# Kernel optimization log

Measured on AMD Instinct MI355X. Metric: run time of the kernel, lower is better.

## Reference

```python
import jax, jax.numpy as jnp
import numpy as np

B, N = 8, 2048
IN_F, MID1, HID, MID2, OUT_F = 128, 128, 128, 128, 128
BIG = 9e15  # matches torch's 9000000000000000.0 additive mask constant


def _linear_params(key, out_d, in_d):
    # torch Linear layout: W is [out, in]
    kw, kb = jax.random.split(key)
    w = jax.random.normal(kw, (out_d, in_d), jnp.float32) * (1.0 / np.sqrt(in_d))
    b = jax.random.normal(kb, (out_d,), jnp.float32) * 0.01
    return w, b


def setup_inputs() -> dict:
    key = jax.random.key(0)
    ks = jax.random.split(key, 16)
    h = jax.random.normal(ks[0], (B, N, IN_F), jnp.float32)
    adj = jax.random.randint(ks[1], (B, N, N), 0, 2).astype(jnp.float32)
    vae2_fetures = jax.random.normal(ks[2], (B, N, OUT_F), jnp.float32)
    Wv1, bv1 = _linear_params(ks[3], MID1, IN_F)
    Wk1, bk1 = _linear_params(ks[4], MID1, IN_F)
    Wq1, bq1 = _linear_params(ks[5], MID1, IN_F)
    Wo1, bo1 = _linear_params(ks[6], HID, MID1)
    Wv2, bv2 = _linear_params(ks[7], MID2, HID)
    Wk2, bk2 = _linear_params(ks[8], MID2, HID)
    Wq2, bq2 = _linear_params(ks[9], MID2, HID)
    Wo2, bo2 = _linear_params(ks[10], OUT_F, MID2)
    Wf, bf = _linear_params(ks[11], OUT_F, 2 * OUT_F)
    return {
        "h": h, "adj": adj, "vae2_fetures": vae2_fetures,
        "Wv1": Wv1, "bv1": bv1, "Wk1": Wk1, "bk1": bk1, "Wq1": Wq1, "bq1": bq1,
        "Wo1": Wo1, "bo1": bo1,
        "Wv2": Wv2, "bv2": bv2, "Wk2": Wk2, "bk2": bk2, "Wq2": Wq2, "bq2": bq2,
        "Wo2": Wo2, "bo2": bo2, "Wf": Wf, "bf": bf,
    }


def _lin(x, W, b):
    return jnp.einsum('bnd,od->bno', x, W) + b


def _masked_att_block(x, adj, Wq, bq, Wk, bk, Wv, bv):
    v = jax.nn.relu(_lin(x, Wv, bv))          # [B,N,D]
    q = jax.nn.relu(_lin(x, Wq, bq))          # [B,N,D]
    k = jax.nn.relu(_lin(x, Wk, bk))          # [B,N,D]
    s = jnp.einsum('bnd,bmd->bnm', q, k)       # [B,N,N]
    masked = s * adj - BIG * (1.0 - adj)       # multiplicative + additive mask
    att = jax.nn.softmax(masked, axis=-1)
    return jnp.einsum('bnm,bmd->bnd', att, v)


def reference(h, adj, vae2_fetures,
              Wv1, bv1, Wk1, bk1, Wq1, bq1, Wo1, bo1,
              Wv2, bv2, Wk2, bk2, Wq2, bq2, Wo2, bo2,
              Wf, bf):
    f1 = _masked_att_block(h, adj, Wq1, bq1, Wk1, bk1, Wv1, bv1)
    f1 = _lin(f1, Wo1, bo1)                    # [B,N,HID]
    f2 = _masked_att_block(f1, adj, Wq2, bq2, Wk2, bk2, Wv2, bv2)
    f2 = _lin(f2, Wo2, bo2)                    # [B,N,OUT_F]
    f3 = jnp.concatenate([f2, vae2_fetures], axis=2)
    return _lin(f3, Wf, bf)                    # [B,N,OUT_F]
```

## Files before the change

kernel.cpp:

```cpp
#include <hip/hip_runtime.h>

typedef short s16x8 __attribute__((ext_vector_type(8)));
typedef float f32x4 __attribute__((ext_vector_type(4)));
typedef unsigned short u16x4v __attribute__((ext_vector_type(4)));

#define NSPLIT 4
#define NROWS 16384
#define MSHIFT 44.0f

__device__ __forceinline__ unsigned short f2bf(float f) {
  union { float fl; unsigned int i; } v; v.fl = f;
  unsigned int x = v.i;
  x += 0x7fffu + ((x >> 16) & 1u);
  return (unsigned short)(x >> 16);
}
__device__ __forceinline__ s16x8 load8_bf16(const unsigned short* p) {
  return *(const s16x8*)p;
}
__device__ __forceinline__ s16x8 load8_f32(const float* p) {
  float4 a = *(const float4*)p;
  float4 b = *(const float4*)(p + 4);
  s16x8 r;
  r[0] = (short)f2bf(a.x); r[1] = (short)f2bf(a.y);
  r[2] = (short)f2bf(a.z); r[3] = (short)f2bf(a.w);
  r[4] = (short)f2bf(b.x); r[5] = (short)f2bf(b.y);
  r[6] = (short)f2bf(b.z); r[7] = (short)f2bf(b.w);
  return r;
}
__device__ __forceinline__ int vperm(int nn) {
  return (nn & ~31) | (((nn >> 2) & 3) << 3) | (((nn >> 4) & 1) << 2);
}

template <int MODE>
__device__ __forceinline__ void qkv_body(
    const float* __restrict__ X, const float* __restrict__ W,
    const float* __restrict__ bias, unsigned short* __restrict__ out)
{
  const int t = threadIdx.x;
  const int w = t >> 6;
  const int lane = t & 63;
  const int l15 = lane & 15;
  const int quad = lane >> 4;
  const int mbase = blockIdx.x * 16;

  s16x8 a[4];
  const float* ar = X + (size_t)(mbase + l15) * 128;
#pragma unroll
  for (int ks = 0; ks < 4; ++ks) a[ks] = load8_f32(ar + ks * 32 + quad * 8);

#pragma unroll
  for (int nt = 0; nt < 2; ++nt) {
    const int n = (w * 2 + nt) * 16 + l15;
    f32x4 acc = {0.f, 0.f, 0.f, 0.f};
    const float* wr = W + (size_t)n * 128;
#pragma unroll
    for (int ks = 0; ks < 4; ++ks)
      acc = __builtin_amdgcn_mfma_f32_16x16x32_bf16(
          a[ks], load8_f32(wr + ks * 32 + quad * 8), acc, 0, 0, 0);
    const float bv = bias[n];
    if (MODE == 0) {
#pragma unroll
      for (int r = 0; r < 4; ++r)
        out[(size_t)(mbase + quad * 4 + r) * 128 + n] = f2bf(fmaxf(acc[r] + bv, 0.f));
    } else {
      const int b  = mbase >> 11;
      const int nn = (mbase & 2047) + quad * 4;
      u16x4v pk;
#pragma unroll
      for (int r = 0; r < 4; ++r) pk[r] = f2bf(fmaxf(acc[r] + bv, 0.f));
      *(u16x4v*)(out + (size_t)(b * 128 + n) * 2048 + vperm(nn)) = pk;
    }
  }
}

__global__ __launch_bounds__(256) void qkv1_kernel(
    const float* __restrict__ x,
    const float* __restrict__ Wq, const float* __restrict__ bq, unsigned short* __restrict__ oq,
    const float* __restrict__ Wk, const float* __restrict__ bk, unsigned short* __restrict__ ok,
    const float* __restrict__ Wv, const float* __restrict__ bv, unsigned short* __restrict__ ovt)
{
  if (blockIdx.y == 0)      qkv_body<0>(x, Wq, bq, oq);
  else if (blockIdx.y == 1) qkv_body<0>(x, Wk, bk, ok);
  else                      qkv_body<1>(x, Wv, bv, ovt);
}

template <bool PACK>
__global__ __launch_bounds__(256, 2) void attn_kernel(
    const unsigned short* __restrict__ Q,
    const unsigned short* __restrict__ K,
    const unsigned short* __restrict__ VT,
    const float* __restrict__ ADJ,
    unsigned long long* __restrict__ MASK,
    float* __restrict__ pO, float* __restrict__ pl)
{
  __shared__ __align__(16) unsigned short kbuf[64][136];
  __shared__ __align__(16) unsigned short vbuf[128][72];

  const int t = threadIdx.x;
  const int w = t >> 6;
  const int lane = t & 63;
  const int l15 = lane & 15;
  const int quad = lane >> 4;

  const int gq0 = blockIdx.x * 128;
  const int b   = gq0 >> 11;
  const int q0  = gq0 & 2047;
  const int wq0 = q0 + w * 32;
  const int kc0 = blockIdx.y * (2048 / NSPLIT);

  const unsigned short* Kb  = K  + (size_t)(b * 2048) * 128;
  const unsigned short* VTb = VT + (size_t)(b * 128) * 2048;
  const float* ADJb = ADJ + (size_t)b * 2048 * 2048;
  unsigned long long* Mb = MASK + (size_t)b * 2048 * 32;

  s16x8 qf[2][4];
#pragma unroll
  for (int mt = 0; mt < 2; ++mt) {
    const unsigned short* qrow = Q + (size_t)(gq0 + w * 32 + mt * 16 + l15) * 128;
#pragma unroll
    for (int ks = 0; ks < 4; ++ks) qf[mt][ks] = load8_bf16(qrow + ks * 32 + quad * 8);
  }

  s16x8 ones;
#pragma unroll
  for (int i = 0; i < 8; ++i) ones[i] = (short)0x3F80;

  f32x4 accO[2][8];
  f32x4 accL[2];
#pragma unroll
  for (int mt = 0; mt < 2; ++mt) {
    accL[mt] = (f32x4){0.f, 0.f, 0.f, 0.f};
#pragma unroll
    for (int dt = 0; dt < 8; ++dt) accO[mt][dt] = (f32x4){0.f, 0.f, 0.f, 0.f};
  }

  s16x8 kr[4], vr[4];
#pragma unroll
  for (int i = 0; i < 4; ++i) {
    int slot = i * 256 + t;
    kr[i] = load8_bf16(Kb + (size_t)(kc0 + (slot >> 4)) * 128 + (slot & 15) * 8);
    vr[i] = load8_bf16(VTb + (size_t)(slot >> 3) * 2048 + kc0 + (slot & 7) * 8);
  }

  for (int kc = kc0; kc < kc0 + 2048 / NSPLIT; kc += 64) {
    __syncthreads();
#pragma unroll
    for (int i = 0; i < 4; ++i) {
      int slot = i * 256 + t;
      *(s16x8*)&kbuf[slot >> 4][(slot & 15) * 8] = kr[i];
      *(s16x8*)&vbuf[slot >> 3][(slot & 7) * 8]  = vr[i];
    }
    __syncthreads();

    unsigned long long mw[2];
    float4 a4[2][4];
    if (PACK) {
#pragma unroll
      for (int mt = 0; mt < 2; ++mt)
#pragma unroll
        for (int nt = 0; nt < 4; ++nt)
          a4[mt][nt] = *(const float4*)(
              ADJb + (size_t)(wq0 + mt * 16 + l15) * 2048 + kc + nt * 16 + quad * 4);
    } else {
#pragma unroll
      for (int mt = 0; mt < 2; ++mt)
        mw[mt] = Mb[(size_t)(wq0 + mt * 16 + l15) * 32 + (kc >> 6)];
    }

    if (kc + 64 < kc0 + 2048 / NSPLIT) {
#pragma unroll
      for (int i = 0; i < 4; ++i) {
        int slot = i * 256 + t;
        kr[i] = load8_bf16(Kb + (size_t)(kc + 64 + (slot >> 4)) * 128 + (slot & 15) * 8);
        vr[i] = load8_bf16(VTb + (size_t)(slot >> 3) * 2048 + (kc + 64) + (slot & 7) * 8);
      }
    }

    f32x4 sv[2][4];
#pragma unroll
    for (int nt = 0; nt < 4; ++nt) {
      sv[0][nt] = (f32x4){0.f, 0.f, 0.f, 0.f};
      sv[1][nt] = (f32x4){0.f, 0.f, 0.f, 0.f};
#pragma unroll
      for (int ks = 0; ks < 4; ++ks) {
        s16x8 kf = *(const s16x8*)&kbuf[nt * 16 + l15][ks * 32 + quad * 8];
        sv[0][nt] = __builtin_amdgcn_mfma_f32_16x16x32_bf16(kf, qf[0][ks], sv[0][nt], 0, 0, 0);
        sv[1][nt] = __builtin_amdgcn_mfma_f32_16x16x32_bf16(kf, qf[1][ks], sv[1][nt], 0, 0, 0);
      }
    }

    float p[2][4][4];
    if (PACK) {
#pragma unroll
      for (int mt = 0; mt < 2; ++mt) {
        unsigned long long word = 0;
#pragma unroll
        for (int nt = 0; nt < 4; ++nt) {
          unsigned int nib = 0;
#pragma unroll
          for (int r = 0; r < 4; ++r) {
            float av = (r == 0) ? a4[mt][nt].x : (r == 1) ? a4[mt][nt].y
                     : (r == 2) ? a4[mt][nt].z : a4[mt][nt].w;
            bool keep = (av != 0.f);
            float e = __expf(sv[mt][nt][r] - MSHIFT);
            p[mt][nt][r] = keep ? e : 0.f;
            nib |= (keep ? 1u : 0u) << r;
          }
          word |= (unsigned long long)nib << (nt * 16 + quad * 4);
        }
        word |= __shfl_xor(word, 16, 64);
        word |= __shfl_xor(word, 32, 64);
        if (quad == 0)
          Mb[(size_t)(wq0 + mt * 16 + l15) * 32 + (kc >> 6)] = word;
      }
    } else {
#pragma unroll
      for (int mt = 0; mt < 2; ++mt)
#pragma unroll
        for (int nt = 0; nt < 4; ++nt)
#pragma unroll
          for (int r = 0; r < 4; ++r) {
            float e = __expf(sv[mt][nt][r] - MSHIFT);
            p[mt][nt][r] = ((mw[mt] >> (nt * 16 + quad * 4 + r)) & 1ull) ? e : 0.f;
          }
    }

    s16x8 pf[2][2];
#pragma unroll
    for (int mt = 0; mt < 2; ++mt)
#pragma unroll
      for (int ks = 0; ks < 2; ++ks) {
        s16x8 v;
#pragma unroll
        for (int j = 0; j < 4; ++j) {
          v[j]     = (short)f2bf(p[mt][2 * ks][j]);
          v[j + 4] = (short)f2bf(p[mt][2 * ks + 1][j]);
        }
        pf[mt][ks] = v;
      }

#pragma unroll
    for (int mt = 0; mt < 2; ++mt)
#pragma unroll
      for (int ks = 0; ks < 2; ++ks)
        accL[mt] = __builtin_amdgcn_mfma_f32_16x16x32_bf16(ones, pf[mt][ks], accL[mt], 0, 0, 0);

#pragma unroll
    for (int dt = 0; dt < 8; ++dt) {
#pragma unroll
      for (int ks = 0; ks < 2; ++ks) {
        s16x8 vf = *(const s16x8*)&vbuf[dt * 16 + l15][ks * 32 + quad * 8];
        accO[0][dt] = __builtin_amdgcn_mfma_f32_16x16x32_bf16(vf, pf[0][ks], accO[0][dt], 0, 0, 0);
        accO[1][dt] = __builtin_amdgcn_mfma_f32_16x16x32_bf16(vf, pf[1][ks], accO[1][dt], 0, 0, 0);
      }
    }
  }

  float* pOs = pO + (size_t)blockIdx.y * NROWS * 128;
#pragma unroll
  for (int mt = 0; mt < 2; ++mt) {
    const int qg = gq0 + w * 32 + mt * 16 + l15;
#pragma unroll
    for (int dt = 0; dt < 8; ++dt)
      *(f32x4*)(pOs + (size_t)qg * 128 + dt * 16 + quad * 4) = accO[mt][dt];
  }
  if (quad == 0) {
#pragma unroll
    for (int mt = 0; mt < 2; ++mt)
      pl[blockIdx.y * NROWS + gq0 + w * 32 + mt * 16 + l15] = accL[mt][0];
  }
}

__device__ __forceinline__ void combine_splits(
    const float* __restrict__ pO, const float* __restrict__ pl, int grow0,
    unsigned short (*At)[136])
{
  const int t = threadIdx.x;
  const int row = t >> 4;
  const int col8 = (t & 15) * 8;
  const int grow = grow0 + row;
  float lsum = 0.f;
#pragma unroll
  for (int s = 0; s < NSPLIT; ++s) lsum += pl[s * NROWS + grow];
  const float inv = (lsum > 0.f) ? 1.f / lsum : 0.f;
  float acc8[8];
#pragma unroll
  for (int i = 0; i < 8; ++i) acc8[i] = 0.f;
#pragma unroll
  for (int s = 0; s < NSPLIT; ++s) {
    const float* p = pO + (size_t)s * NROWS * 128 + (size_t)grow * 128 + col8;
    float4 x0 = *(const float4*)p;
    float4 x1 = *(const float4*)(p + 4);
    acc8[0] += x0.x; acc8[1] += x0.y; acc8[2] += x0.z; acc8[3] += x0.w;
    acc8[4] += x1.x; acc8[5] += x1.y; acc8[6] += x1.z; acc8[7] += x1.w;
  }
#pragma unroll
  for (int i = 0; i < 8; ++i) At[row][col8 + i] = f2bf(acc8[i] * inv);
}

__global__ __launch_bounds__(256) void redqkv_kernel(
    const float* __restrict__ pO, const float* __restrict__ pl,
    const float* __restrict__ Wo, const float* __restrict__ bo,
    const float* __restrict__ Wq, const float* __restrict__ bq, unsigned short* __restrict__ oq,
    const float* __restrict__ Wk, const float* __restrict__ bk, unsigned short* __restrict__ ok,
    const float* __restrict__ Wv, const float* __restrict__ bv, unsigned short* __restrict__ ovt)
{
  __shared__ __align__(16) unsigned short At[16][136];
  __shared__ __align__(16) unsigned short Bt[16][136];
  const int t = threadIdx.x;
  const int grow0 = blockIdx.x * 16;

  combine_splits(pO, pl, grow0, At);
  __syncthreads();

  const int w = t >> 6;
  const int lane = t & 63;
  const int l15 = lane & 15;
  const int quad = lane >> 4;

  s16x8 a[4];
#pragma unroll
  for (int ks = 0; ks < 4; ++ks) a[ks] = *(const s16x8*)&At[l15][ks * 32 + quad * 8];
#pragma unroll
  for (int nt = 0; nt < 2; ++nt) {
    const int n = (w * 2 + nt) * 16 + l15;
    f32x4 acc = {0.f, 0.f, 0.f, 0.f};
    const float* wr = Wo + (size_t)n * 128;
#pragma unroll
    for (int ks = 0; ks < 4; ++ks)
      acc = __builtin_amdgcn_mfma_f32_16x16x32_bf16(
          a[ks], load8_f32(wr + ks * 32 + quad * 8), acc, 0, 0, 0);
    const float bv_ = bo[n];
#pragma unroll
    for (int r = 0; r < 4; ++r) Bt[quad * 4 + r][n] = f2bf(acc[r] + bv_);
  }
  __syncthreads();

  s16x8 a2[4];
#pragma unroll
  for (int ks = 0; ks < 4; ++ks) a2[ks] = *(const s16x8*)&Bt[l15][ks * 32 + quad * 8];

#pragma unroll
  for (int which = 0; which < 3; ++which) {
    const float* W = (which == 0) ? Wq : (which == 1) ? Wk : Wv;
    const float* bb = (which == 0) ? bq : (which == 1) ? bk : bv;
    unsigned short* out = (which == 0) ? oq : (which == 1) ? ok : ovt;
#pragma unroll
    for (int nt = 0; nt < 2; ++nt) {
      const int n = (w * 2 + nt) * 16 + l15;
      f32x4 acc = {0.f, 0.f, 0.f, 0.f};
      const float* wr = W + (size_t)n * 128;
#pragma unroll
      for (int ks = 0; ks < 4; ++ks)
        acc = __builtin_amdgcn_mfma_f32_16x16x32_bf16(
            a2[ks], load8_f32(wr + ks * 32 + quad * 8), acc, 0, 0, 0);
      const float bv_ = bb[n];
      if (which < 2) {
#pragma unroll
        for (int r = 0; r < 4; ++r)
          out[(size_t)(grow0 + quad * 4 + r) * 128 + n] = f2bf(fmaxf(acc[r] + bv_, 0.f));
      } else {
        const int b  = grow0 >> 11;
        const int nn = (grow0 & 2047) + quad * 4;
        u16x4v pk;
#pragma unroll
        for (int r = 0; r < 4; ++r) pk[r] = f2bf(fmaxf(acc[r] + bv_, 0.f));
        *(u16x4v*)(out + (size_t)(b * 128 + n) * 2048 + vperm(nn)) = pk;
      }
    }
  }
}

__global__ __launch_bounds__(256) void redfinal_kernel(
    const float* __restrict__ pO, const float* __restrict__ pl,
    const float* __restrict__ Wo, const float* __restrict__ bo,
    const float* __restrict__ Wf, const float* __restrict__ bff,
    const float* __restrict__ vae2, float* __restrict__ out)
{
  __shared__ __align__(16) unsigned short At[16][136];
  __shared__ __align__(16) unsigned short Bt[16][136];
  const int t = threadIdx.x;
  const int grow0 = blockIdx.x * 16;

  combine_splits(pO, pl, grow0, At);
  __syncthreads();

  const int w = t >> 6;
  const int lane = t & 63;
  const int l15 = lane & 15;
  const int quad = lane >> 4;

  s16x8 a[4];
#pragma unroll
  for (int ks = 0; ks < 4; ++ks) a[ks] = *(const s16x8*)&At[l15][ks * 32 + quad * 8];
#pragma unroll
  for (int nt = 0; nt < 2; ++nt) {
    const int n = (w * 2 + nt) * 16 + l15;
    f32x4 acc = {0.f, 0.f, 0.f, 0.f};
    const float* wr = Wo + (size_t)n * 128;
#pragma unroll
    for (int ks = 0; ks < 4; ++ks)
      acc = __builtin_amdgcn_mfma_f32_16x16x32_bf16(
          a[ks], load8_f32(wr + ks * 32 + quad * 8), acc, 0, 0, 0);
    const float bv_ = bo[n];
#pragma unroll
    for (int r = 0; r < 4; ++r) Bt[quad * 4 + r][n] = f2bf(acc[r] + bv_);
  }
  __syncthreads();

  s16x8 a1[4], a2[4];
#pragma unroll
  for (int ks = 0; ks < 4; ++ks) a1[ks] = *(const s16x8*)&Bt[l15][ks * 32 + quad * 8];
  const float* vrow = vae2 + (size_t)(grow0 + l15) * 128;
#pragma unroll
  for (int ks = 0; ks < 4; ++ks) a2[ks] = load8_f32(vrow + ks * 32 + quad * 8);
#pragma unroll
  for (int nt = 0; nt < 2; ++nt) {
    const int n = (w * 2 + nt) * 16 + l15;
    f32x4 acc = {0.f, 0.f, 0.f, 0.f};
    const float* wr = Wf + (size_t)n * 256;
#pragma unroll
    for (int ks = 0; ks < 4; ++ks)
      acc = __builtin_amdgcn_mfma_f32_16x16x32_bf16(
          a1[ks], load8_f32(wr + ks * 32 + quad * 8), acc, 0, 0, 0);
#pragma unroll
    for (int ks = 0; ks < 4; ++ks)
      acc = __builtin_amdgcn_mfma_f32_16x16x32_bf16(
          a2[ks], load8_f32(wr + 128 + ks * 32 + quad * 8), acc, 0, 0, 0);
    const float bv_ = bff[n];
#pragma unroll
    for (int r = 0; r < 4; ++r)
      out[(size_t)(grow0 + quad * 4 + r) * 128 + n] = acc[r] + bv_;
  }
}

extern "C" void kernel_launch(void* const* d_in, const int* in_sizes, int n_in,
                              void* d_out, int out_size, void* d_ws, size_t ws_size,
                              hipStream_t stream)
{
  const float* h    = (const float*)d_in[0];
  const float* adj  = (const float*)d_in[1];
  const float* vae2 = (const float*)d_in[2];
  const float* Wv1  = (const float*)d_in[3];
  const float* bv1  = (const float*)d_in[4];
  const float* Wk1  = (const float*)d_in[5];
  const float* bk1  = (const float*)d_in[6];
  const float* Wq1  = (const float*)d_in[7];
  const float* bq1  = (const float*)d_in[8];
  const float* Wo1  = (const float*)d_in[9];
  const float* bo1  = (const float*)d_in[10];
  const float* Wv2  = (const float*)d_in[11];
  const float* bv2  = (const float*)d_in[12];
  const float* Wk2  = (const float*)d_in[13];
  const float* bk2  = (const float*)d_in[14];
  const float* Wq2  = (const float*)d_in[15];
  const float* bq2  = (const float*)d_in[16];
  const float* Wo2  = (const float*)d_in[17];
  const float* bo2  = (const float*)d_in[18];
  const float* Wf   = (const float*)d_in[19];
  const float* bff  = (const float*)d_in[20];

  char* wsb = (char*)d_ws;
  const size_t MB = 1u << 20;
  unsigned short* s_q  = (unsigned short*)(wsb + 0 * MB);
  unsigned short* s_k  = (unsigned short*)(wsb + 4 * MB);
  unsigned short* s_vt = (unsigned short*)(wsb + 8 * MB);
  unsigned long long* maskp = (unsigned long long*)(wsb + 12 * MB);
  float* pO = (float*)(wsb + 16 * MB);
  float* pl = (float*)(wsb + 48 * MB);

  qkv1_kernel<<<dim3(1024, 3), dim3(256), 0, stream>>>(
      h, Wq1, bq1, s_q, Wk1, bk1, s_k, Wv1, bv1, s_vt);
  attn_kernel<true><<<dim3(128, NSPLIT), dim3(256), 0, stream>>>(
      s_q, s_k, s_vt, adj, maskp, pO, pl);
  redqkv_kernel<<<dim3(1024), dim3(256), 0, stream>>>(
      pO, pl, Wo1, bo1, Wq2, bq2, s_q, Wk2, bk2, s_k, Wv2, bv2, s_vt);
  attn_kernel<false><<<dim3(128, NSPLIT), dim3(256), 0, stream>>>(
      s_q, s_k, s_vt, nullptr, maskp, pO, pl);
  redfinal_kernel<<<dim3(1024), dim3(256), 0, stream>>>(
      pO, pl, Wo2, bo2, Wf, bff, vae2, (float*)d_out);
}
```

Baseline: 395.5 us.

## Double-buffer attention K/V tiles via direct global-to-LDS loads with XOR swizzle

```diff
diff --git a/kernel.cpp b/kernel.cpp
--- a/kernel.cpp
+++ b/kernel.cpp
@@ -7,6 +7,7 @@
 #define NSPLIT 4
 #define NROWS 16384
 #define MSHIFT 44.0f
+#define NCH (2048 / NSPLIT / 64)
 
 __device__ __forceinline__ unsigned short f2bf(float f) {
   union { float fl; unsigned int i; } v; v.fl = f;
@@ -31,6 +32,12 @@
   return (nn & ~31) | (((nn >> 2) & 3) << 3) | (((nn >> 4) & 1) << 2);
 }
 
+__device__ __forceinline__ void gload16(const void* g, void* l) {
+  __builtin_amdgcn_global_load_lds(
+      (const __attribute__((address_space(1))) void*)g,
+      (__attribute__((address_space(3))) void*)l, 16, 0, 0);
+}
+
 template <int MODE>
 __device__ __forceinline__ void qkv_body(
     const float* __restrict__ X, const float* __restrict__ W,
@@ -93,19 +100,19 @@
     unsigned long long* __restrict__ MASK,
     float* __restrict__ pO, float* __restrict__ pl)
 {
-  __shared__ __align__(16) unsigned short kbuf[64][136];
-  __shared__ __align__(16) unsigned short vbuf[128][72];
+  __shared__ __align__(16) unsigned short kbuf[2][64][128];
+  __shared__ __align__(16) unsigned short vbuf[2][128][64];
 
   const int t = threadIdx.x;
   const int w = t >> 6;
   const int lane = t & 63;
   const int l15 = lane & 15;
   const int quad = lane >> 4;
+  const int x7 = l15 & 7;
 
   const int gq0 = blockIdx.x * 128;
   const int b   = gq0 >> 11;
-  const int q0  = gq0 & 2047;
-  const int wq0 = q0 + w * 32;
+  const int wq0 = (gq0 & 2047) + w * 32;
   const int kc0 = blockIdx.y * (2048 / NSPLIT);
 
   const unsigned short* Kb  = K  + (size_t)(b * 2048) * 128;
@@ -113,6 +120,13 @@
   const float* ADJb = ADJ + (size_t)b * 2048 * 2048;
   unsigned long long* Mb = MASK + (size_t)b * 2048 * 32;
 
+  const int krow = t >> 4;
+  const int kc16 = t & 15;
+  const int kchunk = kc16 ^ (krow & 7);
+  const int vrow = t >> 3;
+  const int vc16 = t & 7;
+  const int vchunk = vc16 ^ (vrow & 7);
+
   s16x8 qf[2][4];
 #pragma unroll
   for (int mt = 0; mt < 2; ++mt) {
@@ -134,45 +148,81 @@
     for (int dt = 0; dt < 8; ++dt) accO[mt][dt] = (f32x4){0.f, 0.f, 0.f, 0.f};
   }
 
-  s16x8 kr[4], vr[4];
-#pragma unroll
-  for (int i = 0; i < 4; ++i) {
-    int slot = i * 256 + t;
-    kr[i] = load8_bf16(Kb + (size_t)(kc0 + (slot >> 4)) * 128 + (slot & 15) * 8);
-    vr[i] = load8_bf16(VTb + (size_t)(slot >> 3) * 2048 + kc0 + (slot & 7) * 8);
-  }
-
-  for (int kc = kc0; kc < kc0 + 2048 / NSPLIT; kc += 64) {
-    __syncthreads();
-#pragma unroll
-    for (int i = 0; i < 4; ++i) {
-      int slot = i * 256 + t;
-      *(s16x8*)&kbuf[slot >> 4][(slot & 15) * 8] = kr[i];
-      *(s16x8*)&vbuf[slot >> 3][(slot & 7) * 8]  = vr[i];
-    }
-    __syncthreads();
-
-    unsigned long long mw[2];
-    float4 a4[2][4];
+#pragma unroll
+  for (int i = 0; i < 4; ++i)
+    gload16(Kb + (size_t)(kc0 + i * 16 + krow) * 128 + kchunk * 8,
+            &kbuf[0][i * 16 + krow][kc16 * 8]);
+#pragma unroll
+  for (int i = 0; i < 4; ++i)
+    gload16(VTb + (size_t)(i * 32 + vrow) * 2048 + kc0 + vchunk * 8,
+            &vbuf[0][i * 32 + vrow][vc16 * 8]);
+
+  float4 a4c[2][4];
+  unsigned long long mwc[2];
+  if (PACK) {
+#pragma unroll
+    for (int mt = 0; mt < 2; ++mt)
+#pragma unroll
+      for (int nt = 0; nt < 4; ++nt)
+        a4c[mt][nt] = *(const float4*)(
+            ADJb + (size_t)(wq0 + mt * 16 + l15) * 2048 + kc0 + nt * 16 + quad * 4);
+  } else {
+#pragma unroll
+    for (int mt = 0; mt < 2; ++mt)
+      mwc[mt] = Mb[(size_t)(wq0 + mt * 16 + l15) * 32 + (kc0 >> 6)];
+  }
+  __syncthreads();
+
+#pragma unroll 2
+  for (int ci = 0; ci < NCH; ++ci) {
+    const int kc = kc0 + ci * 64;
+    unsigned short (*kb)[128] = kbuf[ci & 1];
+    unsigned short (*vb)[64]  = vbuf[ci & 1];
+
+    if (ci + 1 < NCH) {
+      unsigned short (*kbn)[128] = kbuf[(ci + 1) & 1];
+      unsigned short (*vbn)[64]  = vbuf[(ci + 1) & 1];
+#pragma unroll
+      for (int i = 0; i < 4; ++i)
+        gload16(Kb + (size_t)(kc + 64 + i * 16 + krow) * 128 + kchunk * 8,
+                &kbn[i * 16 + krow][kc16 * 8]);
+#pragma unroll
+      for (int i = 0; i < 4; ++i)
+        gload16(VTb + (size_t)(i * 32 + vrow) * 2048 + (kc + 64) + vchunk * 8,
+                &vbn[i * 32 + vrow][vc16 * 8]);
+    }
+
+    unsigned long long kept[2];
     if (PACK) {
 #pragma unroll
-      for (int mt = 0; mt < 2; ++mt)
-#pragma unroll
-        for (int nt = 0; nt < 4; ++nt)
-          a4[mt][nt] = *(const float4*)(
-              ADJb + (size_t)(wq0 + mt * 16 + l15) * 2048 + kc + nt * 16 + quad * 4);
+      for (int mt = 0; mt < 2; ++mt) {
+        unsigned long long word = 0;
+#pragma unroll
+        for (int nt = 0; nt < 4; ++nt) {
+          unsigned int nib = 0;
+          nib |= (a4c[mt][nt].x != 0.f) ? 1u : 0u;
+          nib |= (a4c[mt][nt].y != 0.f) ? 2u : 0u;
+          nib |= (a4c[mt][nt].z != 0.f) ? 4u : 0u;
+          nib |= (a4c[mt][nt].w != 0.f) ? 8u : 0u;
+          word |= (unsigned long long)nib << (nt * 16 + quad * 4);
+        }
+        kept[mt] = word;
+      }
+      if (ci + 1 < NCH) {
+#pragma unroll
+        for (int mt = 0; mt < 2; ++mt)
+#pragma unroll
+          for (int nt = 0; nt < 4; ++nt)
+            a4c[mt][nt] = *(const float4*)(
+                ADJb + (size_t)(wq0 + mt * 16 + l15) * 2048 + (kc + 64) + nt * 16 + quad * 4);
+      }
     } else {
-#pragma unroll
-      for (int mt = 0; mt < 2; ++mt)
-        mw[mt] = Mb[(size_t)(wq0 + mt * 16 + l15) * 32 + (kc >> 6)];
-    }
-
-    if (kc + 64 < kc0 + 2048 / NSPLIT) {
-#pragma unroll
-      for (int i = 0; i < 4; ++i) {
-        int slot = i * 256 + t;
-        kr[i] = load8_bf16(Kb + (size_t)(kc + 64 + (slot >> 4)) * 128 + (slot & 15) * 8);
-        vr[i] = load8_bf16(VTb + (size_t)(slot >> 3) * 2048 + (kc + 64) + (slot & 7) * 8);
+      kept[0] = mwc[0];
+      kept[1] = mwc[1];
+      if (ci + 1 < NCH) {
+#pragma unroll
+        for (int mt = 0; mt < 2; ++mt)
+          mwc[mt] = Mb[(size_t)(wq0 + mt * 16 + l15) * 32 + ((kc + 64) >> 6)];
       }
     }
 
@@ -181,64 +231,54 @@
     for (int nt = 0; nt < 4; ++nt) {
       sv[0][nt] = (f32x4){0.f, 0.f, 0.f, 0.f};
       sv[1][nt] = (f32x4){0.f, 0.f, 0.f, 0.f};
+    }
+    __builtin_amdgcn_s_setprio(1);
+#pragma unroll
+    for (int nt = 0; nt < 4; ++nt)
 #pragma unroll
       for (int ks = 0; ks < 4; ++ks) {
-        s16x8 kf = *(const s16x8*)&kbuf[nt * 16 + l15][ks * 32 + quad * 8];
+        s16x8 kf = *(const s16x8*)&kb[nt * 16 + l15][((ks * 4 + quad) ^ x7) * 8];
         sv[0][nt] = __builtin_amdgcn_mfma_f32_16x16x32_bf16(kf, qf[0][ks], sv[0][nt], 0, 0, 0);
         sv[1][nt] = __builtin_amdgcn_mfma_f32_16x16x32_bf16(kf, qf[1][ks], sv[1][nt], 0, 0, 0);
       }
-    }
-
-    float p[2][4][4];
+    __builtin_amdgcn_s_setprio(0);
+
+    s16x8 pf[2][2];
+#pragma unroll
+    for (int mt = 0; mt < 2; ++mt) {
+      const unsigned int bl = (unsigned int)(kept[mt] >> (quad * 4));
+      const unsigned int bh = (unsigned int)(kept[mt] >> (quad * 4 + 32));
+#pragma unroll
+      for (int ks = 0; ks < 2; ++ks) {
+        s16x8 v;
+#pragma unroll
+        for (int half = 0; half < 2; ++half) {
+          const int nt = ks * 2 + half;
+          const unsigned int bits = (nt < 2) ? bl : bh;
+          const int sh = (nt & 1) * 16;
+#pragma unroll
+          for (int r = 0; r < 4; ++r) {
+            const float e = __expf(sv[mt][nt][r] - MSHIFT);
+            const bool keep = (bits >> (sh + r)) & 1u;
+            v[half * 4 + r] = (short)f2bf(keep ? e : 0.f);
+          }
+        }
+        pf[mt][ks] = v;
+      }
+    }
+
     if (PACK) {
 #pragma unroll
       for (int mt = 0; mt < 2; ++mt) {
-        unsigned long long word = 0;
-#pragma unroll
-        for (int nt = 0; nt < 4; ++nt) {
-          unsigned int nib = 0;
-#pragma unroll
-          for (int r = 0; r < 4; ++r) {
-            float av = (r == 0) ? a4[mt][nt].x : (r == 1) ? a4[mt][nt].y
-                     : (r == 2) ? a4[mt][nt].z : a4[mt][nt].w;
-            bool keep = (av != 0.f);
-            float e = __expf(sv[mt][nt][r] - MSHIFT);
-            p[mt][nt][r] = keep ? e : 0.f;
-            nib |= (keep ? 1u : 0u) << r;
-          }
-          word |= (unsigned long long)nib << (nt * 16 + quad * 4);
-        }
+        unsigned long long word = kept[mt];
         word |= __shfl_xor(word, 16, 64);
         word |= __shfl_xor(word, 32, 64);
         if (quad == 0)
           Mb[(size_t)(wq0 + mt * 16 + l15) * 32 + (kc >> 6)] = word;
       }
-    } else {
-#pragma unroll
-      for (int mt = 0; mt < 2; ++mt)
-#pragma unroll
-        for (int nt = 0; nt < 4; ++nt)
-#pragma unroll
-          for (int r = 0; r < 4; ++r) {
-            float e = __expf(sv[mt][nt][r] - MSHIFT);
-            p[mt][nt][r] = ((mw[mt] >> (nt * 16 + quad * 4 + r)) & 1ull) ? e : 0.f;
-          }
-    }
-
-    s16x8 pf[2][2];
-#pragma unroll
-    for (int mt = 0; mt < 2; ++mt)
-#pragma unroll
-      for (int ks = 0; ks < 2; ++ks) {
-        s16x8 v;
-#pragma unroll
-        for (int j = 0; j < 4; ++j) {
-          v[j]     = (short)f2bf(p[mt][2 * ks][j]);
-          v[j + 4] = (short)f2bf(p[mt][2 * ks + 1][j]);
-        }
-        pf[mt][ks] = v;
-      }
-
+    }
+
+    __builtin_amdgcn_s_setprio(1);
 #pragma unroll
     for (int mt = 0; mt < 2; ++mt)
 #pragma unroll
@@ -246,14 +286,16 @@
         accL[mt] = __builtin_amdgcn_mfma_f32_16x16x32_bf16(ones, pf[mt][ks], accL[mt], 0, 0, 0);
 
 #pragma unroll
-    for (int dt = 0; dt < 8; ++dt) {
+    for (int dt = 0; dt < 8; ++dt)
 #pragma unroll
       for (int ks = 0; ks < 2; ++ks) {
-        s16x8 vf = *(const s16x8*)&vbuf[dt * 16 + l15][ks * 32 + quad * 8];
+        s16x8 vf = *(const s16x8*)&vb[dt * 16 + l15][((ks * 4 + quad) ^ x7) * 8];
         accO[0][dt] = __builtin_amdgcn_mfma_f32_16x16x32_bf16(vf, pf[0][ks], accO[0][dt], 0, 0, 0);
         accO[1][dt] = __builtin_amdgcn_mfma_f32_16x16x32_bf16(vf, pf[1][ks], accO[1][dt], 0, 0, 0);
       }
-    }
+    __builtin_amdgcn_s_setprio(0);
+
+    __syncthreads();
   }
 
   float* pOs = pO + (size_t)blockIdx.y * NROWS * 128;
```

Result: faster. 378.0 us (-4.4%).
